# Performance work log

Hardware: AMD Instinct MI355X
Metric: run time of the kernel (lower is better)

Reference implementation:

```python
import jax, jax.numpy as jnp
import numpy as np

B_SZ, L, H, P = 16, 1024, 256, 256
DT_MIN, DT_MAX = 1e-3, 1e-1


def setup_inputs() -> dict:
    key = jax.random.key(0)
    ks = jax.random.split(key, 6)
    u = jax.random.normal(ks[0], (B_SZ, L, H), dtype=jnp.float32)
    # Stable diagonal init (stands in for HiPPO-LegS diag: negative real part,
    # spread imaginary parts) so exp(Lambda*Delta) has |.|<1 over long scans.
    Lambda_re = -0.5 * jnp.ones((P,), jnp.float32)
    Lambda_im = jnp.pi * jnp.arange(P, dtype=jnp.float32)
    Bp = jax.random.normal(ks[1], (P, H, 2), jnp.float32) / jnp.sqrt(2.0 * H)  # (P,H,2) real/imag
    Cp = jax.random.normal(ks[2], (H, P, 2), jnp.float32) / jnp.sqrt(2.0 * P)  # (H,P,2) real/imag
    D = jax.random.normal(ks[3], (H,), jnp.float32)
    log_step = (jax.random.uniform(ks[4], (P, 1), jnp.float32)
                * (jnp.log(DT_MAX) - jnp.log(DT_MIN)) + jnp.log(DT_MIN))
    return {"u": u, "Lambda_re": Lambda_re, "Lambda_im": Lambda_im,
            "B": Bp, "C": Cp, "D": D, "log_step": log_step}


def _binop(ei, ej):
    # S5 associative scan element: (A, Bu); compose linear recurrences.
    ai, bi = ei
    aj, bj = ej
    return aj * ai, aj * bi + bj


def reference(u, Lambda_re, Lambda_im, B, C, D, log_step):
    # clip_eigs=False, step_rescale=1.0, conj_sym=True, discretization='zoh'
    Lambda = Lambda_re + 1j * Lambda_im                     # (P,) complex
    B_tilde = B[..., 0] + 1j * B[..., 1]                    # (P,H) complex
    C_tilde = C[..., 0] + 1j * C[..., 1]                    # (H,P) complex
    Delta = jnp.exp(log_step[:, 0])                         # (P,)
    # ZOH discretization
    Lambda_bar = jnp.exp(Lambda * Delta)                    # (P,)
    B_bar = ((Lambda_bar - 1.0) / Lambda)[:, None] * B_tilde  # (P,H)
    # Input projection: (B, L, P) complex
    Bu = jnp.einsum('ph,blh->blp', B_bar, u.astype(B_bar.dtype))
    Lam = jnp.broadcast_to(Lambda_bar, Bu.shape)            # (B, L, P)
    # Parallel associative scan over time axis
    _, xs = jax.lax.associative_scan(_binop, (Lam, Bu), axis=1)  # states (B,L,P)
    # Output projection; conj_sym -> 2 * real part
    ys = 2.0 * jnp.einsum('hp,blp->blh', C_tilde, xs).real  # (B,L,H)
    return ys + D * u                                       # feedthrough
```

## Files before the change

### kernel.cpp

```cpp
#include <hip/hip_runtime.h>
#include <hip/hip_bf16.h>
#include <math.h>

#define BB     16
#define LSEQ   1024
#define HH     256
#define PP     256
#define MROWS  (BB*LSEQ)
#define LC     32
#define NC     (LSEQ/LC)
#define NCHUNK (BB*NC)

#define OFF_W1T  0u
#define OFF_W2T  262144u
#define OFF_PW   524288u
#define OFF_CEND 655360u
#define OFF_XS   1703936u

#define XSTRIDE 520

typedef __attribute__((ext_vector_type(8))) short short8;
typedef __attribute__((ext_vector_type(4))) float floatx4;

__device__ __forceinline__ float bf2f(unsigned hs) {
    union { unsigned u; float f; } v; v.u = hs << 16; return v.f;
}
__device__ __forceinline__ unsigned short f2bs(float f) {
    __hip_bfloat16 h = __float2bfloat16(f);
    union { __hip_bfloat16 h; unsigned short s; } v; v.h = h; return v.s;
}
__device__ __forceinline__ unsigned packbf(float r, float i) {
    return (unsigned)f2bs(r) | ((unsigned)f2bs(i) << 16);
}
__device__ __forceinline__ void async16(const void* g, void* l) {
    __builtin_amdgcn_global_load_lds(
        (const __attribute__((address_space(1))) unsigned*)g,
        (__attribute__((address_space(3))) unsigned*)l, 16, 0, 0);
}
__device__ __forceinline__ float2 lam_pow(float lr, float li, float dtt) {
    float m = expf(lr * dtt);
    return make_float2(m * cosf(li * dtt), m * sinf(li * dtt));
}

__global__ void k_prep(const float* __restrict__ Bm, const float* __restrict__ Cm,
                       const float* __restrict__ Lr, const float* __restrict__ Li,
                       const float* __restrict__ ls, char* __restrict__ ws) {
    int blk = blockIdx.x, t = threadIdx.x;
    if (blk < 256) {
        int p = blk, h = t;
        float lr = Lr[p], li = Li[p];
        float dt = expf(ls[p]);
        float2 lam = lam_pow(lr, li, dt);
        float den = lr * lr + li * li;
        float nr = lam.x - 1.0f, ni = lam.y;
        float cr = (nr * lr + ni * li) / den;
        float ci = (ni * lr - nr * li) / den;
        float br = Bm[(p * HH + h) * 2 + 0];
        float bi = Bm[(p * HH + h) * 2 + 1];
        unsigned short* w1 = (unsigned short*)(ws + OFF_W1T);
        w1[(2 * p) * 256 + h]     = f2bs(cr * br - ci * bi);
        w1[(2 * p + 1) * 256 + h] = f2bs(cr * bi + ci * br);
        if (t <= 32)
            ((float2*)(ws + OFF_PW))[t * 256 + p] = lam_pow(lr, li, dt * (float)t);
    } else {
        int h = blk - 256, p = t;
        float c_r = Cm[(h * PP + p) * 2 + 0];
        float c_i = Cm[(h * PP + p) * 2 + 1];
        ((unsigned*)(ws + OFF_W2T))[h * 256 + p] = packbf(2.0f * c_r, -2.0f * c_i);
    }
}

__global__ __launch_bounds__(512, 4) void k_g1scan(
        const float* __restrict__ u, const float* __restrict__ Lr,
        const float* __restrict__ Li, const float* __restrict__ ls,
        char* __restrict__ ws) {
    __shared__ char smem[2048 + 33280];
    unsigned*  As32 = (unsigned*)smem;
    char*      Bs   = smem + 2048;
    unsigned short* X = (unsigned short*)(smem + 2048);
    unsigned*  X32  = (unsigned*)(smem + 2048);
    const unsigned short* W1 = (const unsigned short*)(ws + OFF_W1T);
    const int tid = threadIdx.x, bc = blockIdx.x;
    const int wave = tid >> 6, lane = tid & 63;
    const int q = lane >> 4, rr = lane & 15;
    const int c4 = lane & 3, r4 = lane >> 2;
    const int m0 = bc * LC;

    floatx4 acc[2][4];
    #pragma unroll
    for (int i = 0; i < 2; ++i)
        #pragma unroll
        for (int j = 0; j < 4; ++j) acc[i][j] = (floatx4)0.0f;

    const int urow = tid >> 4, ucol2 = (tid & 15) * 2;
    for (int k0 = 0; k0 < 256; k0 += 32) {
        __syncthreads();
        float2 v = *(const float2*)(u + (size_t)(m0 + urow) * 256 + k0 + ucol2);
        As32[urow * 16 + (tid & 15)] = packbf(v.x, v.y);
        #pragma unroll
        for (int t = wave; t < 32; t += 8)
            async16(W1 + (size_t)(t * 16 + r4) * 256 + k0 + c4 * 8,
                    Bs + t * 1024 + lane * 16);
        __syncthreads();
        short8 a0 = *(const short8*)((char*)As32 + rr * 64 + q * 16);
        short8 a1 = *(const short8*)((char*)As32 + (16 + rr) * 64 + q * 16);
        #pragma unroll
        for (int j = 0; j < 4; ++j) {
            short8 b = *(const short8*)(Bs + ((wave * 4 + j) * 16 + rr) * 64 + q * 16);
            acc[0][j] = __builtin_amdgcn_mfma_f32_16x16x32_bf16(a0, b, acc[0][j], 0, 0, 0);
            acc[1][j] = __builtin_amdgcn_mfma_f32_16x16x32_bf16(a1, b, acc[1][j], 0, 0, 0);
        }
    }
    __syncthreads();
    #pragma unroll
    for (int i = 0; i < 2; ++i)
        #pragma unroll
        for (int j = 0; j < 4; ++j)
            #pragma unroll
            for (int r0 = 0; r0 < 4; ++r0)
                X[(i * 16 + q * 4 + r0) * XSTRIDE + wave * 64 + j * 16 + rr] =
                    f2bs(acc[i][j][r0]);
    __syncthreads();

    if (tid < 256) {
        const int p = tid;
        const float2 lam = lam_pow(Lr[p], Li[p], expf(ls[p]));
        unsigned* xs32 = (unsigned*)(ws + OFF_XS);
        float xr = 0.0f, xi = 0.0f;
        for (int j = 0; j < LC; ++j) {
            unsigned cv = X32[j * (XSTRIDE / 2) + p];
            float br = bf2f(cv & 0xffffu), bi = bf2f(cv >> 16);
            float nr = fmaf(lam.x, xr, fmaf(-lam.y, xi, br));
            float ni = fmaf(lam.x, xi, fmaf(lam.y, xr, bi));
            xr = nr; xi = ni;
            xs32[(size_t)(m0 + j) * 256 + p] = packbf(xr, xi);
        }
        ((float2*)(ws + OFF_CEND))[bc * 256 + p] = make_float2(xr, xi);
    }
}

__global__ __launch_bounds__(256, 2) void k_gemm2fix(
        const char* __restrict__ ws_c, const float* __restrict__ D,
        const float* __restrict__ u, float* __restrict__ out,
        const float* __restrict__ Lr, const float* __restrict__ Li,
        const float* __restrict__ ls) {
    __shared__ unsigned short As[64 * 32];
    __shared__ unsigned short Bs[128 * 32];
    __shared__ float2 carr[2][256];
    const unsigned short* W2 = (const unsigned short*)(ws_c + OFF_W2T);
    const unsigned* xs32 = (const unsigned*)(ws_c + OFF_XS);
    const float2* pw = (const float2*)(ws_c + OFF_PW);
    const float2* cend = (const float2*)(ws_c + OFF_CEND);

    const int tid = threadIdx.x;
    const int wave = tid >> 6, lane = tid & 63;
    const int q = lane >> 4, rr = lane & 15;
    const int c4 = lane & 3, r4 = lane >> 2;
    const int wm = wave & 1, wn = wave >> 1;
    const int m0 = blockIdx.y * 64, n0 = blockIdx.x * 128;
    const int b = m0 >> 10;
    const int c = (m0 >> 5) & 31;

    {
        const int p = tid;
        const float dt = expf(ls[p]);
        const float2 g = lam_pow(Lr[p], Li[p], dt * (float)LC);
        float sr = 0.0f, si = 0.0f;
        for (int cc = 0; cc < c; ++cc) {
            float2 e = cend[(size_t)(b * NC + cc) * 256 + p];
            float nr = fmaf(g.x, sr, fmaf(-g.y, si, e.x));
            float ni = fmaf(g.x, si, fmaf(g.y, sr, e.y));
            sr = nr; si = ni;
        }
        carr[0][p] = make_float2(sr, si);
        float2 e = cend[(size_t)(b * NC + c) * 256 + p];
        carr[1][p] = make_float2(fmaf(g.x, sr, fmaf(-g.y, si, e.x)),
                                 fmaf(g.x, si, fmaf(g.y, sr, e.y)));
    }

    floatx4 acc[2][4];
    #pragma unroll
    for (int i = 0; i < 2; ++i)
        #pragma unroll
        for (int j = 0; j < 4; ++j) acc[i][j] = (floatx4)0.0f;

    const int sr_ = tid & 63;
    const int qd  = tid >> 6;
    const int grow = m0 + sr_;
    const int jj = (grow & (LC - 1)) + 1;
    const int half = sr_ >> 5;

    for (int k0 = 0; k0 < 512; k0 += 32) {
        __syncthreads();
        {
            int p0 = (k0 >> 1) + qd * 4;
            uint4 xv = *(const uint4*)(xs32 + (size_t)grow * 256 + p0);
            float4 pw01 = *(const float4*)(pw + (size_t)jj * 256 + p0);
            float4 pw23 = *(const float4*)(pw + (size_t)jj * 256 + p0 + 2);
            float4 ca01 = *(const float4*)(&carr[half][p0]);
            float4 ca23 = *(const float4*)(&carr[half][p0 + 2]);
            unsigned o0 = packbf(bf2f(xv.x & 0xffffu) + (pw01.x * ca01.x - pw01.y * ca01.y),
                                 bf2f(xv.x >> 16)     + (pw01.x * ca01.y + pw01.y * ca01.x));
            unsigned o1 = packbf(bf2f(xv.y & 0xffffu) + (pw01.z * ca01.z - pw01.w * ca01.w),
                                 bf2f(xv.y >> 16)     + (pw01.z * ca01.w + pw01.w * ca01.z));
            unsigned o2 = packbf(bf2f(xv.z & 0xffffu) + (pw23.x * ca23.x - pw23.y * ca23.y),
                                 bf2f(xv.z >> 16)     + (pw23.x * ca23.y + pw23.y * ca23.x));
            unsigned o3 = packbf(bf2f(xv.w & 0xffffu) + (pw23.z * ca23.z - pw23.w * ca23.w),
                                 bf2f(xv.w >> 16)     + (pw23.z * ca23.w + pw23.w * ca23.z));
            *(uint4*)((char*)As + sr_ * 64 + qd * 16) = make_uint4(o0, o1, o2, o3);
        }
        #pragma unroll
        for (int t = wave; t < 8; t += 4)
            async16(W2 + (size_t)(n0 + t * 16 + r4) * 512 + k0 + c4 * 8,
                    (char*)Bs + t * 1024 + lane * 16);
        __syncthreads();
        short8 a[2], bfrag[4];
        #pragma unroll
        for (int i = 0; i < 2; ++i)
            a[i] = *(const short8*)((const char*)As + ((wm * 2 + i) * 16 + rr) * 64 + q * 16);
        #pragma unroll
        for (int j = 0; j < 4; ++j)
            bfrag[j] = *(const short8*)((const char*)Bs + ((wn * 4 + j) * 16 + rr) * 64 + q * 16);
        #pragma unroll
        for (int i = 0; i < 2; ++i)
            #pragma unroll
            for (int j = 0; j < 4; ++j)
                acc[i][j] = __builtin_amdgcn_mfma_f32_16x16x32_bf16(a[i], bfrag[j], acc[i][j], 0, 0, 0);
    }

    #pragma unroll
    for (int i = 0; i < 2; ++i) {
        int mbase = m0 + wm * 32 + i * 16 + q * 4;
        #pragma unroll
        for (int j = 0; j < 4; ++j) {
            int col = n0 + wn * 64 + j * 16 + rr;
            #pragma unroll
            for (int r0 = 0; r0 < 4; ++r0) {
                int row = mbase + r0;
                size_t gi = (size_t)row * 256 + col;
                out[gi] = acc[i][j][r0] + D[col] * u[gi];
            }
        }
    }
}

extern "C" void kernel_launch(void* const* d_in, const int* in_sizes, int n_in,
                              void* d_out, int out_size, void* d_ws, size_t ws_size,
                              hipStream_t stream) {
    const float* u  = (const float*)d_in[0];
    const float* Lr = (const float*)d_in[1];
    const float* Li = (const float*)d_in[2];
    const float* Bm = (const float*)d_in[3];
    const float* Cm = (const float*)d_in[4];
    const float* D  = (const float*)d_in[5];
    const float* ls = (const float*)d_in[6];
    float* out = (float*)d_out;
    char* ws = (char*)d_ws;

    k_prep<<<512, 256, 0, stream>>>(Bm, Cm, Lr, Li, ls, ws);
    k_g1scan<<<NCHUNK, 512, 0, stream>>>(u, Lr, Li, ls, ws);
    k_gemm2fix<<<dim3(2, MROWS / 64), 256, 0, stream>>>(ws, D, u, out, Lr, Li, ls);
}
```

Baseline: 123.2 us.

## Precompute chunk carries in separate kernel and double K-step of both GEMMs

Moves the sequential inter-chunk carry recurrence out of the output GEMM into a small dedicated kernel that writes per-chunk prefix states to workspace. Each GEMM block now only loads two carry vectors instead of redoing up to 31 serial steps. Both GEMM loops also process 64-wide K slices as two 32-wide panels per synchronisation, which halves barrier count but doubles shared memory in the scan kernel and lowers its occupancy bound. The change adds one extra kernel launch and a workspace round trip for the carries.

```diff
diff --git a/kernel.cpp b/kernel.cpp
--- a/kernel.cpp
+++ b/kernel.cpp
@@ -15,7 +15,8 @@
 #define OFF_W2T  262144u
 #define OFF_PW   524288u
 #define OFF_CEND 655360u
-#define OFF_XS   1703936u
+#define OFF_CARR 1703936u
+#define OFF_XS   2752512u
 
 #define XSTRIDE 520
 
@@ -70,15 +71,15 @@
     }
 }
 
-__global__ __launch_bounds__(512, 4) void k_g1scan(
+__global__ __launch_bounds__(512, 2) void k_g1scan(
         const float* __restrict__ u, const float* __restrict__ Lr,
         const float* __restrict__ Li, const float* __restrict__ ls,
         char* __restrict__ ws) {
-    __shared__ char smem[2048 + 33280];
-    unsigned*  As32 = (unsigned*)smem;
-    char*      Bs   = smem + 2048;
-    unsigned short* X = (unsigned short*)(smem + 2048);
-    unsigned*  X32  = (unsigned*)(smem + 2048);
+    __shared__ char smem[4096 + 65536];
+    char* Asb = smem;
+    char* Bsb = smem + 4096;
+    unsigned short* X = (unsigned short*)smem;
+    unsigned* X32 = (unsigned*)smem;
     const unsigned short* W1 = (const unsigned short*)(ws + OFF_W1T);
     const int tid = threadIdx.x, bc = blockIdx.x;
     const int wave = tid >> 6, lane = tid & 63;
@@ -92,23 +93,33 @@
         #pragma unroll
         for (int j = 0; j < 4; ++j) acc[i][j] = (floatx4)0.0f;
 
-    const int urow = tid >> 4, ucol2 = (tid & 15) * 2;
-    for (int k0 = 0; k0 < 256; k0 += 32) {
-        __syncthreads();
-        float2 v = *(const float2*)(u + (size_t)(m0 + urow) * 256 + k0 + ucol2);
-        As32[urow * 16 + (tid & 15)] = packbf(v.x, v.y);
-        #pragma unroll
-        for (int t = wave; t < 32; t += 8)
-            async16(W1 + (size_t)(t * 16 + r4) * 256 + k0 + c4 * 8,
-                    Bs + t * 1024 + lane * 16);
-        __syncthreads();
-        short8 a0 = *(const short8*)((char*)As32 + rr * 64 + q * 16);
-        short8 a1 = *(const short8*)((char*)As32 + (16 + rr) * 64 + q * 16);
-        #pragma unroll
-        for (int j = 0; j < 4; ++j) {
-            short8 b = *(const short8*)(Bs + ((wave * 4 + j) * 16 + rr) * 64 + q * 16);
-            acc[0][j] = __builtin_amdgcn_mfma_f32_16x16x32_bf16(a0, b, acc[0][j], 0, 0, 0);
-            acc[1][j] = __builtin_amdgcn_mfma_f32_16x16x32_bf16(a1, b, acc[1][j], 0, 0, 0);
+    const int arow = tid >> 4, acol4 = (tid & 15) * 4;
+    const int apan = acol4 >> 5, acin = acol4 & 31;
+    for (int k0 = 0; k0 < 256; k0 += 64) {
+        __syncthreads();
+        float4 v = *(const float4*)(u + (size_t)(m0 + arow) * 256 + k0 + acol4);
+        *(uint2*)(Asb + apan * 2048 + arow * 64 + acin * 2) =
+            make_uint2(packbf(v.x, v.y), packbf(v.z, v.w));
+        #pragma unroll
+        for (int t = 0; t < 8; ++t) {
+            int idx = t * 8 + wave;
+            int pan = idx & 1, rowg = idx >> 1;
+            int row = rowg * 16 + r4;
+            async16(W1 + (size_t)row * 256 + k0 + pan * 32 + c4 * 8,
+                    Bsb + pan * 32768 + row * 64 + c4 * 16);
+        }
+        __syncthreads();
+        #pragma unroll
+        for (int ks = 0; ks < 2; ++ks) {
+            short8 a0 = *(const short8*)(Asb + ks * 2048 + rr * 64 + q * 16);
+            short8 a1 = *(const short8*)(Asb + ks * 2048 + (16 + rr) * 64 + q * 16);
+            #pragma unroll
+            for (int j = 0; j < 4; ++j) {
+                short8 b = *(const short8*)(Bsb + ks * 32768 +
+                                            ((wave * 4 + j) * 16 + rr) * 64 + q * 16);
+                acc[0][j] = __builtin_amdgcn_mfma_f32_16x16x32_bf16(a0, b, acc[0][j], 0, 0, 0);
+                acc[1][j] = __builtin_amdgcn_mfma_f32_16x16x32_bf16(a1, b, acc[1][j], 0, 0, 0);
+            }
         }
     }
     __syncthreads();
@@ -139,18 +150,34 @@
     }
 }
 
-__global__ __launch_bounds__(256, 2) void k_gemm2fix(
+__global__ void k_carry(const float* __restrict__ Lr, const float* __restrict__ Li,
+                        const float* __restrict__ ls, char* __restrict__ ws) {
+    int p = threadIdx.x, b = blockIdx.x;
+    float dt = expf(ls[p]);
+    float2 g = lam_pow(Lr[p], Li[p], dt * (float)LC);
+    const float2* cend = (const float2*)(ws + OFF_CEND);
+    float2* carr = (float2*)(ws + OFF_CARR);
+    float sr = 0.0f, si = 0.0f;
+    for (int c = 0; c < NC; ++c) {
+        size_t off = (size_t)(b * NC + c) * 256 + p;
+        carr[off] = make_float2(sr, si);
+        float2 e = cend[off];
+        float nr = fmaf(g.x, sr, fmaf(-g.y, si, e.x));
+        float ni = fmaf(g.x, si, fmaf(g.y, sr, e.y));
+        sr = nr; si = ni;
+    }
+}
+
+__global__ __launch_bounds__(256, 4) void k_gemm2fix(
         const char* __restrict__ ws_c, const float* __restrict__ D,
-        const float* __restrict__ u, float* __restrict__ out,
-        const float* __restrict__ Lr, const float* __restrict__ Li,
-        const float* __restrict__ ls) {
-    __shared__ unsigned short As[64 * 32];
-    __shared__ unsigned short Bs[128 * 32];
-    __shared__ float2 carr[2][256];
+        const float* __restrict__ u, float* __restrict__ out) {
+    __shared__ char Asb[8192];
+    __shared__ char Bsb[16384];
+    __shared__ float2 carrs[2][256];
     const unsigned short* W2 = (const unsigned short*)(ws_c + OFF_W2T);
     const unsigned* xs32 = (const unsigned*)(ws_c + OFF_XS);
     const float2* pw = (const float2*)(ws_c + OFF_PW);
-    const float2* cend = (const float2*)(ws_c + OFF_CEND);
+    const float2* carr = (const float2*)(ws_c + OFF_CARR);
 
     const int tid = threadIdx.x;
     const int wave = tid >> 6, lane = tid & 63;
@@ -158,24 +185,11 @@
     const int c4 = lane & 3, r4 = lane >> 2;
     const int wm = wave & 1, wn = wave >> 1;
     const int m0 = blockIdx.y * 64, n0 = blockIdx.x * 128;
-    const int b = m0 >> 10;
-    const int c = (m0 >> 5) & 31;
 
     {
-        const int p = tid;
-        const float dt = expf(ls[p]);
-        const float2 g = lam_pow(Lr[p], Li[p], dt * (float)LC);
-        float sr = 0.0f, si = 0.0f;
-        for (int cc = 0; cc < c; ++cc) {
-            float2 e = cend[(size_t)(b * NC + cc) * 256 + p];
-            float nr = fmaf(g.x, sr, fmaf(-g.y, si, e.x));
-            float ni = fmaf(g.x, si, fmaf(g.y, sr, e.y));
-            sr = nr; si = ni;
-        }
-        carr[0][p] = make_float2(sr, si);
-        float2 e = cend[(size_t)(b * NC + c) * 256 + p];
-        carr[1][p] = make_float2(fmaf(g.x, sr, fmaf(-g.y, si, e.x)),
-                                 fmaf(g.x, si, fmaf(g.y, sr, e.y)));
+        int cbase = m0 >> 5;
+        carrs[0][tid] = carr[(size_t)cbase * 256 + tid];
+        carrs[1][tid] = carr[(size_t)(cbase + 1) * 256 + tid];
     }
 
     floatx4 acc[2][4];
@@ -184,48 +198,59 @@
         #pragma unroll
         for (int j = 0; j < 4; ++j) acc[i][j] = (floatx4)0.0f;
 
-    const int sr_ = tid & 63;
-    const int qd  = tid >> 6;
-    const int grow = m0 + sr_;
+    const int row = tid >> 2, qd = tid & 3;
+    const int grow = m0 + row;
     const int jj = (grow & (LC - 1)) + 1;
-    const int half = sr_ >> 5;
-
-    for (int k0 = 0; k0 < 512; k0 += 32) {
+    const int half = row >> 5;
+
+    for (int k0 = 0; k0 < 512; k0 += 64) {
         __syncthreads();
         {
-            int p0 = (k0 >> 1) + qd * 4;
-            uint4 xv = *(const uint4*)(xs32 + (size_t)grow * 256 + p0);
-            float4 pw01 = *(const float4*)(pw + (size_t)jj * 256 + p0);
-            float4 pw23 = *(const float4*)(pw + (size_t)jj * 256 + p0 + 2);
-            float4 ca01 = *(const float4*)(&carr[half][p0]);
-            float4 ca23 = *(const float4*)(&carr[half][p0 + 2]);
-            unsigned o0 = packbf(bf2f(xv.x & 0xffffu) + (pw01.x * ca01.x - pw01.y * ca01.y),
-                                 bf2f(xv.x >> 16)     + (pw01.x * ca01.y + pw01.y * ca01.x));
-            unsigned o1 = packbf(bf2f(xv.y & 0xffffu) + (pw01.z * ca01.z - pw01.w * ca01.w),
-                                 bf2f(xv.y >> 16)     + (pw01.z * ca01.w + pw01.w * ca01.z));
-            unsigned o2 = packbf(bf2f(xv.z & 0xffffu) + (pw23.x * ca23.x - pw23.y * ca23.y),
-                                 bf2f(xv.z >> 16)     + (pw23.x * ca23.y + pw23.y * ca23.x));
-            unsigned o3 = packbf(bf2f(xv.w & 0xffffu) + (pw23.z * ca23.z - pw23.w * ca23.w),
-                                 bf2f(xv.w >> 16)     + (pw23.z * ca23.w + pw23.w * ca23.z));
-            *(uint4*)((char*)As + sr_ * 64 + qd * 16) = make_uint4(o0, o1, o2, o3);
-        }
-        #pragma unroll
-        for (int t = wave; t < 8; t += 4)
-            async16(W2 + (size_t)(n0 + t * 16 + r4) * 512 + k0 + c4 * 8,
-                    (char*)Bs + t * 1024 + lane * 16);
-        __syncthreads();
-        short8 a[2], bfrag[4];
-        #pragma unroll
-        for (int i = 0; i < 2; ++i)
-            a[i] = *(const short8*)((const char*)As + ((wm * 2 + i) * 16 + rr) * 64 + q * 16);
-        #pragma unroll
-        for (int j = 0; j < 4; ++j)
-            bfrag[j] = *(const short8*)((const char*)Bs + ((wn * 4 + j) * 16 + rr) * 64 + q * 16);
-        #pragma unroll
-        for (int i = 0; i < 2; ++i)
+            int p0 = (k0 >> 1) + qd * 8;
+            uint4 xa = *(const uint4*)(xs32 + (size_t)grow * 256 + p0);
+            uint4 xb = *(const uint4*)(xs32 + (size_t)grow * 256 + p0 + 4);
+            unsigned xv[8] = {xa.x, xa.y, xa.z, xa.w, xb.x, xb.y, xb.z, xb.w};
+            const float2* pwp = pw + (size_t)jj * 256 + p0;
+            const float2* cap = &carrs[half][p0];
+            unsigned o[8];
+            #pragma unroll
+            for (int e = 0; e < 8; ++e) {
+                float2 pwv = pwp[e];
+                float2 cav = cap[e];
+                float fr = pwv.x * cav.x - pwv.y * cav.y;
+                float fi = pwv.x * cav.y + pwv.y * cav.x;
+                o[e] = packbf(bf2f(xv[e] & 0xffffu) + fr, bf2f(xv[e] >> 16) + fi);
+            }
+            char* dst = Asb + (qd >> 1) * 4096 + row * 64 + (qd & 1) * 32;
+            *(uint4*)dst        = make_uint4(o[0], o[1], o[2], o[3]);
+            *(uint4*)(dst + 16) = make_uint4(o[4], o[5], o[6], o[7]);
+        }
+        #pragma unroll
+        for (int t = 0; t < 4; ++t) {
+            int idx = t * 4 + wave;
+            int pan = idx & 1, rowg = idx >> 1;
+            int rw = rowg * 16 + r4;
+            async16(W2 + (size_t)(n0 + rw) * 512 + k0 + pan * 32 + c4 * 8,
+                    Bsb + pan * 8192 + rw * 64 + c4 * 16);
+        }
+        __syncthreads();
+        #pragma unroll
+        for (int ks = 0; ks < 2; ++ks) {
+            short8 a[2], bfr[4];
+            #pragma unroll
+            for (int i = 0; i < 2; ++i)
+                a[i] = *(const short8*)(Asb + ks * 4096 +
+                                        (wm * 32 + i * 16 + rr) * 64 + q * 16);
             #pragma unroll
             for (int j = 0; j < 4; ++j)
-                acc[i][j] = __builtin_amdgcn_mfma_f32_16x16x32_bf16(a[i], bfrag[j], acc[i][j], 0, 0, 0);
+                bfr[j] = *(const short8*)(Bsb + ks * 8192 +
+                                          ((wn * 64 + j * 16 + rr)) * 64 + q * 16);
+            #pragma unroll
+            for (int i = 0; i < 2; ++i)
+                #pragma unroll
+                for (int j = 0; j < 4; ++j)
+                    acc[i][j] = __builtin_amdgcn_mfma_f32_16x16x32_bf16(a[i], bfr[j], acc[i][j], 0, 0, 0);
+        }
     }
 
     #pragma unroll
@@ -236,8 +261,8 @@
             int col = n0 + wn * 64 + j * 16 + rr;
             #pragma unroll
             for (int r0 = 0; r0 < 4; ++r0) {
-                int row = mbase + r0;
-                size_t gi = (size_t)row * 256 + col;
+                int rw = mbase + r0;
+                size_t gi = (size_t)rw * 256 + col;
                 out[gi] = acc[i][j][r0] + D[col] * u[gi];
             }
         }
@@ -259,5 +284,6 @@
 
     k_prep<<<512, 256, 0, stream>>>(Bm, Cm, Lr, Li, ls, ws);
     k_g1scan<<<NCHUNK, 512, 0, stream>>>(u, Lr, Li, ls, ws);
-    k_gemm2fix<<<dim3(2, MROWS / 64), 256, 0, stream>>>(ws, D, u, out, Lr, Li, ls);
-}
+    k_carry<<<BB, 256, 0, stream>>>(Lr, Li, ls, ws);
+    k_gemm2fix<<<dim3(2, MROWS / 64), 256, 0, stream>>>(ws, D, u, out);
+}
```

New measurement: 115.0 us. -6.7%, faster.
